# Optimization experiments

Hardware: AMD Instinct MI355X
Metric: run time of the kernel (lower is better)

Reference implementation:

```python
import jax, jax.numpy as jnp
import numpy as np

D = 512
HEAD_NUMB = 8

def setup_inputs() -> dict:
    key = jax.random.key(0)
    k1, k2, k3 = jax.random.split(key, 3)
    x = jax.random.normal(k1, (4, 4096, D), dtype=jnp.float32)
    # nn.Linear(D, 3D): weight [3D, D], bias [3D]
    W_qkv = jax.random.normal(k2, (3 * D, D), dtype=jnp.float32) / np.sqrt(D)
    b_qkv = jax.random.normal(k3, (3 * D,), dtype=jnp.float32) * 0.01
    return {"x": x, "W_qkv": W_qkv, "b_qkv": b_qkv}

def reference(x, W_qkv, b_qkv):
    # fused QKV projection: x @ W^T + b  -> [B, N, 3D]
    qkv = jnp.einsum('bnd,ed->bne', x, W_qkv) + b_qkv
    q = qkv[:, :, :D]
    k = qkv[:, :, D:2 * D]
    v = qkv[:, :, 2 * D:]
    scaling = (D / HEAD_NUMB) ** (-0.5)
    # single-head attention over full D (faithful to the original module)
    scores = jnp.einsum('bqd,bkd->bqk', q, k) * scaling  # [B, N, N]
    attn = jax.nn.softmax(scores, axis=2)
    return jnp.einsum('bqk,bkd->bqd', attn, v)
```

## Files before the change

### kernel.cpp

```cpp
#include <hip/hip_runtime.h>
#include <hip/hip_bf16.h>

#define D_DIM 512
#define NSEQ  4096
#define BATCH 4
#define SCALE 0.125f

typedef __attribute__((ext_vector_type(8)))  short short8;
typedef __attribute__((ext_vector_type(16))) float floatx16;

__device__ __forceinline__ unsigned short f2bf(float f) {
    __hip_bfloat16 h = __float2bfloat16(f);
    return *reinterpret_cast<unsigned short*>(&h);
}

__device__ __forceinline__ floatx16 mfma_bf16(short8 a, short8 b, floatx16 c) {
    return __builtin_amdgcn_mfma_f32_32x32x16_bf16(a, b, c, 0, 0, 0);
}

#define GLOAD16(g, l) __builtin_amdgcn_global_load_lds( \
    (const __attribute__((address_space(1))) unsigned int*)(g), \
    (__attribute__((address_space(3))) unsigned int*)(l), 16, 0, 0)

__global__ __launch_bounds__(256) void cast_inputs(
    const float* __restrict__ x, const float* __restrict__ W,
    unsigned short* __restrict__ xb, unsigned short* __restrict__ Wb)
{
    const size_t NX = (size_t)BATCH * NSEQ * D_DIM;
    size_t i = ((size_t)blockIdx.x * 256 + threadIdx.x) * 8;
    const float* src; unsigned short* dst;
    if (i < NX) { src = x + i; dst = xb + i; }
    else        { src = W + (i - NX); dst = Wb + (i - NX); }
    float4 v0 = *(const float4*)(src);
    float4 v1 = *(const float4*)(src + 4);
    short8 h;
    h[0] = (short)f2bf(v0.x); h[1] = (short)f2bf(v0.y);
    h[2] = (short)f2bf(v0.z); h[3] = (short)f2bf(v0.w);
    h[4] = (short)f2bf(v1.x); h[5] = (short)f2bf(v1.y);
    h[6] = (short)f2bf(v1.z); h[7] = (short)f2bf(v1.w);
    *(short8*)dst = h;
}

__global__ __launch_bounds__(256, 2) void qkv_gemm(
    const unsigned short* __restrict__ xb, const unsigned short* __restrict__ Wb,
    const float* __restrict__ bias,
    unsigned short* __restrict__ qs, unsigned short* __restrict__ kk,
    unsigned short* __restrict__ vT)
{
    __shared__ __align__(16) unsigned short S2[2][128 * 64];
    unsigned short* Xs = S2[0];
    unsigned short* Ws = S2[1];
    unsigned short* Tr = &S2[0][0];

    const int t = threadIdx.x;
    const int lane = t & 63, w = t >> 6;
    const int l31 = lane & 31, lh = lane >> 5;
    const int wm = w >> 1, we = w & 1;
    const int n0 = blockIdx.x * 128;
    const int m0 = blockIdx.y * 128;

    floatx16 a00, a01, a10, a11;
#pragma unroll
    for (int r = 0; r < 16; r++) { a00[r] = 0.f; a01[r] = 0.f; a10[r] = 0.f; a11[r] = 0.f; }

    int rowp[4], colp[4];
#pragma unroll
    for (int p = 0; p < 4; p++) {
        int o = p * 4096 + t * 16;
        int row = o >> 7;
        int sl  = ((o >> 4) & 7) ^ (row & 7);
        rowp[p] = row; colp[p] = sl * 8;
    }

    for (int kc = 0; kc < 8; kc++) {
        const int k0 = kc * 64;
        __syncthreads();
#pragma unroll
        for (int p = 0; p < 4; p++) {
            GLOAD16(xb + (size_t)(m0 + rowp[p]) * D_DIM + k0 + colp[p],
                    (char*)Xs + p * 4096 + (t & ~63) * 16);
            GLOAD16(Wb + (size_t)(n0 + rowp[p]) * D_DIM + k0 + colp[p],
                    (char*)Ws + p * 4096 + (t & ~63) * 16);
        }
        __syncthreads();
        const int sw = l31 & 7;
#pragma unroll
        for (int ks = 0; ks < 4; ks++) {
            const int s = ks * 2 + lh;
            const int cof = ((s ^ sw) * 8);
            short8 fa0 = *(const short8*)&Xs[(wm * 64 +      l31) * 64 + cof];
            short8 fa1 = *(const short8*)&Xs[(wm * 64 + 32 + l31) * 64 + cof];
            short8 fb0 = *(const short8*)&Ws[(we * 64 +      l31) * 64 + cof];
            short8 fb1 = *(const short8*)&Ws[(we * 64 + 32 + l31) * 64 + cof];
            a00 = mfma_bf16(fa0, fb0, a00);
            a01 = mfma_bf16(fa0, fb1, a01);
            a10 = mfma_bf16(fa1, fb0, a10);
            a11 = mfma_bf16(fa1, fb1, a11);
        }
    }

    if (n0 < 1024) {
#pragma unroll
        for (int jt = 0; jt < 2; jt++) {
            const int e = n0 + we * 64 + jt * 32 + l31;
            const float bv = bias[e];
#pragma unroll
            for (int it = 0; it < 2; it++) {
                const int mb = m0 + wm * 64 + it * 32;
                const floatx16& av = (it == 0) ? ((jt == 0) ? a00 : a01)
                                               : ((jt == 0) ? a10 : a11);
                if (e < 512) {
#pragma unroll
                    for (int r = 0; r < 16; r++) {
                        int m = mb + (r & 3) + 8 * (r >> 2) + 4 * lh;
                        qs[(size_t)m * D_DIM + e] = f2bf((av[r] + bv) * SCALE);
                    }
                } else {
#pragma unroll
                    for (int r = 0; r < 16; r++) {
                        int m = mb + (r & 3) + 8 * (r >> 2) + 4 * lh;
                        kk[(size_t)m * D_DIM + (e - 512)] = f2bf(av[r] + bv);
                    }
                }
            }
        }
    } else {
        __syncthreads();
#pragma unroll
        for (int jt = 0; jt < 2; jt++) {
            const int dd = we * 64 + jt * 32 + l31;
            const float bv = bias[n0 + dd];
#pragma unroll
            for (int it = 0; it < 2; it++) {
                const floatx16& av = (it == 0) ? ((jt == 0) ? a00 : a01)
                                               : ((jt == 0) ? a10 : a11);
#pragma unroll
                for (int q = 0; q < 4; q++) {
                    int tt = wm * 64 + it * 32 + 8 * q + 4 * lh;
                    ushort4 hv;
                    hv.x = f2bf(av[4 * q + 0] + bv); hv.y = f2bf(av[4 * q + 1] + bv);
                    hv.z = f2bf(av[4 * q + 2] + bv); hv.w = f2bf(av[4 * q + 3] + bv);
                    int byte = dd * 256 + ((((tt >> 3) ^ (dd & 7)) << 4)) + ((tt & 7) << 1);
                    *(ushort4*)((char*)Tr + byte) = hv;
                }
            }
        }
        __syncthreads();
        const int rown = t >> 4;
        const int c    = t & 15;
        const int bb = m0 >> 12, tok0 = (m0 & 4095);
#pragma unroll
        for (int g = 0; g < 8; g++) {
            int row = g * 16 + rown;
            int byte = row * 256 + ((c ^ (row & 7)) << 4);
            uint4 v = *(const uint4*)((char*)Tr + byte);
            *(uint4*)(vT + ((size_t)bb * 512 + (n0 - 1024) + row) * 4096
                      + tok0 + c * 8) = v;
        }
    }
}

#define FA_BQ 64
#define FA_BK 256
#define FA_DC 128
#define QC_STR 136
#define KC_STR 136
#define P_STR  264
#define VT2_STR 40

__global__ __launch_bounds__(512, 1) void flash_attn(
    const unsigned short* __restrict__ qs, const unsigned short* __restrict__ kk,
    const unsigned short* __restrict__ vT, float* __restrict__ out)
{
    __shared__ __align__(16) unsigned char smem[123392];
    unsigned short* Qc = (unsigned short*)(smem);
    unsigned short* Kc = (unsigned short*)(smem + 17408);
    unsigned short* Vt = (unsigned short*)(smem);
    unsigned short* P  = (unsigned short*)(smem + 87040);
    float* pmax    = (float*)(smem + 120832);
    float* psum    = (float*)(smem + 121856);
    float* alpha_s = (float*)(smem + 122880);
    float* l_s     = (float*)(smem + 123136);

    const int t = threadIdx.x;
    const int lane = t & 63, w = t >> 6;
    const int l31 = lane & 31, lh = lane >> 5;
    const int wi = w & 1, wjj = w >> 1;
    const int b  = blockIdx.y;
    const int q0 = blockIdx.x * FA_BQ;
    const size_t qbase = ((size_t)b * NSEQ + q0) * D_DIM;
    const size_t kbase = (size_t)b * NSEQ * D_DIM;
    const size_t vbase = (size_t)b * D_DIM * NSEQ;

    const int i_my = wi * 32 + l31;

    const int vd[4] = { (t + 0) >> 2, (t + 512) >> 2, (t + 1024) >> 2, (t + 1536) >> 2 };
    const int vc = (t & 3) * 8;

    uint4 rv[4];

#define ISSUE_V32(kt_, jc8_) do {                                             \
    _Pragma("unroll")                                                         \
    for (int p = 0; p < 4; p++)                                               \
        rv[p] = *(const uint4*)(vT + vbase + (size_t)vd[p] * NSEQ             \
                                + (kt_) + (jc8_) * 32 + vc);                  \
} while (0)

#define WRITE_V32(buf_) do {                                                  \
    _Pragma("unroll")                                                         \
    for (int p = 0; p < 4; p++)                                               \
        *(uint4*)&Vt[(buf_) * 20480 + vd[p] * VT2_STR + vc] = rv[p];          \
} while (0)

    floatx16 o00, o01, o10, o11;
#pragma unroll
    for (int r = 0; r < 16; r++) { o00[r] = 0.f; o01[r] = 0.f; o10[r] = 0.f; o11[r] = 0.f; }
    float m_st = -__builtin_inff(), l_st = 0.f;

    for (int kt = 0; kt < NSEQ; kt += FA_BK) {
        floatx16 s0, s1;
#pragma unroll
        for (int r = 0; r < 16; r++) { s0[r] = 0.f; s1[r] = 0.f; }

        for (int dc = 0; dc < D_DIM; dc += FA_DC) {
            __syncthreads();
#pragma unroll
            for (int p = 0; p < 2; p++) {
                int id = t + p * 512;
                int row = id >> 4, c8 = id & 15;
                uint4 v = *(const uint4*)(qs + qbase + (size_t)row * D_DIM + dc + c8 * 8);
                *(uint4*)&Qc[row * QC_STR + c8 * 8] = v;
            }
#pragma unroll
            for (int p = 0; p < 8; p++) {
                int id = t + p * 512;
                int row = id >> 4, c8 = id & 15;
                uint4 v = *(const uint4*)(kk + kbase + (size_t)(kt + row) * D_DIM + dc + c8 * 8);
                *(uint4*)&Kc[row * KC_STR + c8 * 8] = v;
            }
            __syncthreads();
            const unsigned short* kr0 = &Kc[(wjj * 64 + l31) * KC_STR];
            const unsigned short* kr1 = kr0 + 32 * KC_STR;
            const unsigned short* qr  = &Qc[i_my * QC_STR];
            __builtin_amdgcn_s_setprio(1);
#pragma unroll
            for (int ks = 0; ks < 8; ks++) {
                const int co = ks * 16 + lh * 8;
                short8 fa0 = *(const short8*)(kr0 + co);
                short8 fa1 = *(const short8*)(kr1 + co);
                short8 fb  = *(const short8*)(qr + co);
                s0 = mfma_bf16(fa0, fb, s0);
                s1 = mfma_bf16(fa1, fb, s1);
            }
            __builtin_amdgcn_s_setprio(0);
        }

        ISSUE_V32(kt, 0);

        float mx = -__builtin_inff();
#pragma unroll
        for (int r = 0; r < 16; r++) mx = fmaxf(mx, fmaxf(s0[r], s1[r]));
        mx = fmaxf(mx, __shfl_xor(mx, 32));
        if (lh == 0) pmax[i_my * 4 + wjj] = mx;
        __syncthreads();
        float4 pm = *(float4*)&pmax[i_my * 4];
        const float m_new = fmaxf(m_st, fmaxf(fmaxf(pm.x, pm.y), fmaxf(pm.z, pm.w)));
        const float alpha = __expf(m_st - m_new);
        m_st = m_new;

        float sum = 0.f;
        {
            const int prow = i_my * P_STR;
#pragma unroll
            for (int q = 0; q < 4; q++) {
                float p0 = __expf(s0[4*q+0] - m_new), p1 = __expf(s0[4*q+1] - m_new);
                float p2 = __expf(s0[4*q+2] - m_new), p3 = __expf(s0[4*q+3] - m_new);
                sum += (p0 + p1) + (p2 + p3);
                ushort4 h; h.x = f2bf(p0); h.y = f2bf(p1); h.z = f2bf(p2); h.w = f2bf(p3);
                *(ushort4*)&P[prow + (wjj*2+0)*32 + 8*q + 4*lh] = h;
            }
#pragma unroll
            for (int q = 0; q < 4; q++) {
                float p0 = __expf(s1[4*q+0] - m_new), p1 = __expf(s1[4*q+1] - m_new);
                float p2 = __expf(s1[4*q+2] - m_new), p3 = __expf(s1[4*q+3] - m_new);
                sum += (p0 + p1) + (p2 + p3);
                ushort4 h; h.x = f2bf(p0); h.y = f2bf(p1); h.z = f2bf(p2); h.w = f2bf(p3);
                *(ushort4*)&P[prow + (wjj*2+1)*32 + 8*q + 4*lh] = h;
            }
        }
        sum += __shfl_xor(sum, 32);
        if (lh == 0) psum[i_my * 4 + wjj] = sum;
        if (lh == 0 && wjj == 0) alpha_s[i_my] = alpha;
        WRITE_V32(0);
        __syncthreads();
        float4 ps = *(float4*)&psum[i_my * 4];
        l_st = l_st * alpha + ((ps.x + ps.y) + (ps.z + ps.w));

        float av[2][16];
        bool ch = false;
#pragma unroll
        for (int it = 0; it < 2; it++)
#pragma unroll
            for (int q = 0; q < 4; q++) {
                float4 a4 = *(float4*)&alpha_s[it * 32 + 8 * q + 4 * lh];
                av[it][4*q+0] = a4.x; av[it][4*q+1] = a4.y;
                av[it][4*q+2] = a4.z; av[it][4*q+3] = a4.w;
                ch = ch || (a4.x != 1.f) || (a4.y != 1.f) || (a4.z != 1.f) || (a4.w != 1.f);
            }
        if (__any(ch)) {
#pragma unroll
            for (int r = 0; r < 16; r++) {
                o00[r] *= av[0][r]; o01[r] *= av[0][r];
                o10[r] *= av[1][r]; o11[r] *= av[1][r];
            }
        }

#pragma unroll
        for (int p8 = 0; p8 < 8; p8++) {
            if (p8 > 0) {
                WRITE_V32(p8 & 1);
                __syncthreads();
            }
            if (p8 < 7) ISSUE_V32(kt, p8 + 1);
            const unsigned short* pr0 = &P[l31 * P_STR + p8 * 32];
            const unsigned short* pr1 = &P[(32 + l31) * P_STR + p8 * 32];
            const unsigned short* vr0 = &Vt[(p8 & 1) * 20480 + (w * 64 + l31) * VT2_STR];
            const unsigned short* vr1 = vr0 + 32 * VT2_STR;
            __builtin_amdgcn_s_setprio(1);
#pragma unroll
            for (int js = 0; js < 2; js++) {
                const int co = js * 16 + lh * 8;
                short8 pa0 = *(const short8*)(pr0 + co);
                short8 pa1 = *(const short8*)(pr1 + co);
                short8 vb0 = *(const short8*)(vr0 + co);
                short8 vb1 = *(const short8*)(vr1 + co);
                o00 = mfma_bf16(pa0, vb0, o00);
                o01 = mfma_bf16(pa0, vb1, o01);
                o10 = mfma_bf16(pa1, vb0, o10);
                o11 = mfma_bf16(pa1, vb1, o11);
            }
            __builtin_amdgcn_s_setprio(0);
        }
    }

    if (lh == 0 && wjj == 0) l_s[i_my] = l_st;
    __syncthreads();
    float iv[2][16];
#pragma unroll
    for (int it = 0; it < 2; it++)
#pragma unroll
        for (int q = 0; q < 4; q++) {
            float4 l4 = *(float4*)&l_s[it * 32 + 8 * q + 4 * lh];
            iv[it][4*q+0] = 1.f / l4.x; iv[it][4*q+1] = 1.f / l4.y;
            iv[it][4*q+2] = 1.f / l4.z; iv[it][4*q+3] = 1.f / l4.w;
        }
#pragma unroll
    for (int it = 0; it < 2; it++) {
        const floatx16& oa = (it == 0) ? o00 : o10;
        const floatx16& ob = (it == 0) ? o01 : o11;
#pragma unroll
        for (int r = 0; r < 16; r++) {
            const int i = it * 32 + (r & 3) + 8 * (r >> 2) + 4 * lh;
            const size_t rowb = ((size_t)b * NSEQ + q0 + i) * D_DIM;
            out[rowb + w * 64 + l31]      = oa[r] * iv[it][r];
            out[rowb + w * 64 + 32 + l31] = ob[r] * iv[it][r];
        }
    }
#undef ISSUE_V32
#undef WRITE_V32
}

extern "C" void kernel_launch(void* const* d_in, const int* in_sizes, int n_in,
                              void* d_out, int out_size, void* d_ws, size_t ws_size,
                              hipStream_t stream)
{
    (void)in_sizes; (void)n_in; (void)out_size; (void)ws_size;
    const float* x    = (const float*)d_in[0];
    const float* W    = (const float*)d_in[1];
    const float* bias = (const float*)d_in[2];
    float* out = (float*)d_out;

    unsigned short* qs = (unsigned short*)d_ws;
    unsigned short* kk = qs + (size_t)16384 * 512;
    unsigned short* vT = kk + (size_t)16384 * 512;
    unsigned short* xb = vT + (size_t)BATCH * D_DIM * NSEQ;
    unsigned short* Wb = xb + (size_t)16384 * 512;

    cast_inputs<<<dim3(4480), 256, 0, stream>>>(x, W, xb, Wb);
    qkv_gemm<<<dim3(12, 128), 256, 0, stream>>>(xb, Wb, bias, qs, kk, vT);
    flash_attn<<<dim3(NSEQ / FA_BQ, BATCH), 512, 0, stream>>>(qs, kk, vT, out);
}
```

Measured before the change: 410.9 us.

## Replace register-prefetched double-buffered V staging with synchronous 64-wide chunks

Removes the register prefetch of V tiles that overlapped global loads with the P·V MFMAs across 8 double-buffered 32-column chunks. It now loads 4 larger 64-column V chunks directly into a single LDS buffer between barriers. The launch bound moves to 2 blocks per CU, aiming to hide latency through occupancy instead of software pipelining. The risks are exposed load latency, since loads are no longer overlapped, and register pressure. The shared memory footprint of about 123 KB may also still block two resident blocks.

```diff
diff --git a/kernel.cpp b/kernel.cpp
--- a/kernel.cpp
+++ b/kernel.cpp
@@ -166,9 +166,9 @@
 #define QC_STR 136
 #define KC_STR 136
 #define P_STR  264
-#define VT2_STR 40
-
-__global__ __launch_bounds__(512, 1) void flash_attn(
+#define VT_STR 72
+
+__global__ __launch_bounds__(512, 2) void flash_attn(
     const unsigned short* __restrict__ qs, const unsigned short* __restrict__ kk,
     const unsigned short* __restrict__ vT, float* __restrict__ out)
 {
@@ -194,24 +194,6 @@
 
     const int i_my = wi * 32 + l31;
 
-    const int vd[4] = { (t + 0) >> 2, (t + 512) >> 2, (t + 1024) >> 2, (t + 1536) >> 2 };
-    const int vc = (t & 3) * 8;
-
-    uint4 rv[4];
-
-#define ISSUE_V32(kt_, jc8_) do {                                             \
-    _Pragma("unroll")                                                         \
-    for (int p = 0; p < 4; p++)                                               \
-        rv[p] = *(const uint4*)(vT + vbase + (size_t)vd[p] * NSEQ             \
-                                + (kt_) + (jc8_) * 32 + vc);                  \
-} while (0)
-
-#define WRITE_V32(buf_) do {                                                  \
-    _Pragma("unroll")                                                         \
-    for (int p = 0; p < 4; p++)                                               \
-        *(uint4*)&Vt[(buf_) * 20480 + vd[p] * VT2_STR + vc] = rv[p];          \
-} while (0)
-
     floatx16 o00, o01, o10, o11;
 #pragma unroll
     for (int r = 0; r < 16; r++) { o00[r] = 0.f; o01[r] = 0.f; o10[r] = 0.f; o11[r] = 0.f; }
@@ -255,8 +237,6 @@
             __builtin_amdgcn_s_setprio(0);
         }
 
-        ISSUE_V32(kt, 0);
-
         float mx = -__builtin_inff();
 #pragma unroll
         for (int r = 0; r < 16; r++) mx = fmaxf(mx, fmaxf(s0[r], s1[r]));
@@ -291,7 +271,6 @@
         sum += __shfl_xor(sum, 32);
         if (lh == 0) psum[i_my * 4 + wjj] = sum;
         if (lh == 0 && wjj == 0) alpha_s[i_my] = alpha;
-        WRITE_V32(0);
         __syncthreads();
         float4 ps = *(float4*)&psum[i_my * 4];
         l_st = l_st * alpha + ((ps.x + ps.y) + (ps.z + ps.w));
@@ -315,20 +294,23 @@
             }
         }
 
-#pragma unroll
-        for (int p8 = 0; p8 < 8; p8++) {
-            if (p8 > 0) {
-                WRITE_V32(p8 & 1);
-                __syncthreads();
-            }
-            if (p8 < 7) ISSUE_V32(kt, p8 + 1);
-            const unsigned short* pr0 = &P[l31 * P_STR + p8 * 32];
-            const unsigned short* pr1 = &P[(32 + l31) * P_STR + p8 * 32];
-            const unsigned short* vr0 = &Vt[(p8 & 1) * 20480 + (w * 64 + l31) * VT2_STR];
-            const unsigned short* vr1 = vr0 + 32 * VT2_STR;
+        for (int jc = 0; jc < 4; jc++) {
+            __syncthreads();
+#pragma unroll
+            for (int p = 0; p < 8; p++) {
+                int id = t + p * 512;
+                int d = id >> 3, c8 = id & 7;
+                uint4 v = *(const uint4*)(vT + vbase + (size_t)d * NSEQ + kt + jc * 64 + c8 * 8);
+                *(uint4*)&Vt[d * VT_STR + c8 * 8] = v;
+            }
+            __syncthreads();
+            const unsigned short* pr0 = &P[l31 * P_STR + jc * 64];
+            const unsigned short* pr1 = &P[(32 + l31) * P_STR + jc * 64];
+            const unsigned short* vr0 = &Vt[(w * 64 + l31) * VT_STR];
+            const unsigned short* vr1 = vr0 + 32 * VT_STR;
             __builtin_amdgcn_s_setprio(1);
 #pragma unroll
-            for (int js = 0; js < 2; js++) {
+            for (int js = 0; js < 4; js++) {
                 const int co = js * 16 + lh * 8;
                 short8 pa0 = *(const short8*)(pr0 + co);
                 short8 pa1 = *(const short8*)(pr1 + co);
@@ -366,8 +348,6 @@
             out[rowb + w * 64 + 32 + l31] = ob[r] * iv[it][r];
         }
     }
-#undef ISSUE_V32
-#undef WRITE_V32
 }
 
 extern "C" void kernel_launch(void* const* d_in, const int* in_sizes, int n_in,
```

After: 357.2 us. 1.15x faster.
